# Performance work log

Measured on AMD Instinct MI355X. Metric: run time of the kernel, lower is better.

The kernel has to match this reference:

```python
import jax, jax.numpy as jnp
import numpy as np

EMBD = 256
HEAD = 4
HEAD_DIM = EMBD // HEAD  # 64


def setup_inputs() -> dict:
    key = jax.random.key(0)
    ks = jax.random.split(key, 5)
    B, S = 16, 1024
    scale = 1.0 / np.sqrt(EMBD)
    return {
        "x": jax.random.normal(ks[0], (B, S, EMBD), dtype=jnp.float32),
        "W_qkv": jax.random.normal(ks[1], (EMBD, 3 * EMBD), dtype=jnp.float32) * scale,
        "b_qkv": jax.random.normal(ks[2], (3 * EMBD,), dtype=jnp.float32) * 0.01,
        "W_out": jax.random.normal(ks[3], (EMBD, EMBD), dtype=jnp.float32) * scale,
        "b_out": jax.random.normal(ks[4], (EMBD,), dtype=jnp.float32) * 0.01,
    }


def reference(x, W_qkv, b_qkv, W_out, b_out):
    B, S, E = x.shape
    qkv = x @ W_qkv + b_qkv  # [B,S,3E]
    q, k, v = jnp.split(qkv, 3, axis=-1)
    # [B,S,E] -> [B,H,S,D]
    q = q.reshape(B, S, HEAD, HEAD_DIM).transpose(0, 2, 1, 3)
    k = k.reshape(B, S, HEAD, HEAD_DIM).transpose(0, 2, 1, 3)
    v = v.reshape(B, S, HEAD, HEAD_DIM).transpose(0, 2, 1, 3)
    att = jnp.einsum("bhqd,bhkd->bhqk", q, k) / jnp.sqrt(jnp.float32(HEAD_DIM))
    causal = jnp.tril(jnp.ones((S, S), dtype=bool))
    att = jnp.where(causal, att, -jnp.inf)
    att = jax.nn.softmax(att, axis=-1)
    out = jnp.einsum("bhqk,bhkd->bhqd", att, v)  # [B,H,S,D]
    out = out.transpose(0, 2, 1, 3).reshape(B, S, E)
    return out @ W_out + b_out
```

## Files before the change

kernel.cpp:

```cpp
#include <hip/hip_runtime.h>


typedef unsigned short ushort_t;
typedef __bf16 bf16x8 __attribute__((ext_vector_type(8)));
typedef __bf16 bf16x4 __attribute__((ext_vector_type(4)));
typedef unsigned short u16x8 __attribute__((ext_vector_type(8)));
typedef unsigned short u16x4 __attribute__((ext_vector_type(4)));
typedef float f32x4 __attribute__((ext_vector_type(4)));
typedef short s16x4 __attribute__((ext_vector_type(4)));

__device__ __forceinline__ ushort_t f2bf(float f) {
  __bf16 h = (__bf16)f;
  return __builtin_bit_cast(ushort_t, h);
}

__device__ __forceinline__ void gload_lds16(const ushort_t* g, ushort_t* l) {
  __builtin_amdgcn_global_load_lds(
      (const __attribute__((address_space(1))) unsigned int*)g,
      (__attribute__((address_space(3))) unsigned int*)l, 16, 0, 0);
}

#define BARRIER_RAW() do { __builtin_amdgcn_s_barrier(); \
                           __builtin_amdgcn_sched_barrier(0); } while (0)

__device__ __forceinline__ f32x4 mfma16(bf16x4 a, bf16x4 b, f32x4 c) {
#if __has_builtin(__builtin_amdgcn_mfma_f32_16x16x16bf16_1k)
  return __builtin_amdgcn_mfma_f32_16x16x16bf16_1k(
      __builtin_bit_cast(s16x4, a), __builtin_bit_cast(s16x4, b), c, 0, 0, 0);
#elif __has_builtin(__builtin_amdgcn_mfma_f32_16x16x16_bf16)
  return __builtin_amdgcn_mfma_f32_16x16x16_bf16(a, b, c, 0, 0, 0);
#else
  f32x4 d = c;
  asm volatile("v_mfma_f32_16x16x16_bf16 %0, %1, %2, %0"
               : "+v"(d) : "v"(a), "v"(b));
  return d;
#endif
}

__global__ __launch_bounds__(256)
void convert_all(const float* __restrict__ x,
                 const float* __restrict__ Wq, const float* __restrict__ Wo,
                 ushort_t* __restrict__ xb,
                 ushort_t* __restrict__ WqT, ushort_t* __restrict__ WoT)
{
  int blk = blockIdx.x;
  if (blk < 2048) {
    const int xc = blk & 7, j = blk >> 3;
    const size_t base = (size_t)xc * 524288 + (size_t)j * 2048 + threadIdx.x * 8;
    float4 v0 = *(const float4*)&x[base];
    float4 v1 = *(const float4*)&x[base + 4];
    u16x8 ov;
    ov[0]=f2bf(v0.x); ov[1]=f2bf(v0.y); ov[2]=f2bf(v0.z); ov[3]=f2bf(v0.w);
    ov[4]=f2bf(v1.x); ov[5]=f2bf(v1.y); ov[6]=f2bf(v1.z); ov[7]=f2bf(v1.w);
    *(u16x8*)&xb[base] = ov;
    return;
  }
  blk -= 2048;
  __shared__ float t[64][65];
  const float* src; ushort_t* dst; int ld_src, k0, n0;
  if (blk < 48) { src = Wq; dst = WqT; ld_src = 768;
                  k0 = (blk / 12) * 64; n0 = (blk % 12) * 64; }
  else { blk -= 48; src = Wo; dst = WoT; ld_src = 256;
         k0 = (blk / 4) * 64; n0 = (blk % 4) * 64; }
  const int tr = threadIdx.x >> 6, tc = threadIdx.x & 63;
  #pragma unroll
  for (int i = 0; i < 16; ++i) {
    const int r = i * 4 + tr;
    t[r][tc] = src[(size_t)(k0 + r) * ld_src + n0 + tc];
  }
  __syncthreads();
  #pragma unroll
  for (int i = 0; i < 16; ++i) {
    const int r = i * 4 + tr;
    dst[(size_t)(n0 + r) * 256 + k0 + tc] = f2bf(t[tc][r]);
  }
}

template<int OUT_MODE, int NB>
__global__ __launch_bounds__(256, 2)
void gemm_bias(const ushort_t* __restrict__ A, int ldA,
               const ushort_t* __restrict__ Bt,
               const float* __restrict__ bias,
               void* __restrict__ Outp, int ldOut,
               ushort_t* __restrict__ Vt)
{
  __shared__ ushort_t Bl[64][256];
  __shared__ ushort_t Al[4][3][64][32];

  const int tid = threadIdx.x;
  const int lane = tid & 63;
  const int w  = tid >> 6;
  const int l15 = lane & 15, g = lane >> 4;

  const int nwg = NB * 64;
  const int inner = (int)blockIdx.x % nwg;
  const int chunkXCD = nwg >> 3;
  const int gidx = (inner & 7) * chunkXCD + (inner >> 3);
  const int n0 = (gidx % NB) * 64;
  const int mBase = (gidx / NB) * 256;
  const int mw = mBase + w * 64;
  const bool vmode = (OUT_MODE == 0) && (n0 >= 512);

  #pragma unroll
  for (int i = 0; i < 8; ++i) {
    const int L = i * 256 + tid;
    const int r = L >> 5, c = L & 31;
    gload_lds16(&Bt[(size_t)(n0 + r) * 256 + (c ^ (r & 7)) * 8],
                &Bl[0][0] + (size_t)L * 8);
  }
  #pragma unroll
  for (int s = 0; s < 2; ++s)
    #pragma unroll
    for (int i = 0; i < 4; ++i) {
      const int L = i * 64 + lane;
      const int r = L >> 2, c = L & 3;
      gload_lds16(&A[(size_t)(mw + r) * ldA + s*32 + (c ^ ((r >> 1) & 3)) * 8],
                  &Al[w][s][0][0] + (size_t)L * 8);
    }
  asm volatile("s_waitcnt vmcnt(8)" ::: "memory");
  BARRIER_RAW();

  f32x4 acc[4][4] = {};

  #pragma unroll
  for (int t = 0; t < 8; ++t) {
    if (t < 6) {
      #pragma unroll
      for (int i = 0; i < 4; ++i) {
        const int L = i * 64 + lane;
        const int r = L >> 2, c = L & 3;
        gload_lds16(&A[(size_t)(mw + r) * ldA + (t+2)*32
                       + (c ^ ((r >> 1) & 3)) * 8],
                    &Al[w][(t + 2) % 3][0][0] + (size_t)L * 8);
      }
    }
    if (t < 6)      asm volatile("s_waitcnt vmcnt(8)" ::: "memory");
    else if (t == 6) asm volatile("s_waitcnt vmcnt(4)" ::: "memory");
    else             asm volatile("s_waitcnt vmcnt(0)" ::: "memory");

    bf16x8 af[4], bfr[4];
    #pragma unroll
    for (int mi = 0; mi < 4; ++mi) {
      const int r = mi * 16 + l15;
      af[mi] = __builtin_bit_cast(bf16x8,
          *(const u16x8*)&Al[w][t % 3][r][(g ^ ((r >> 1) & 3)) * 8]);
    }
    #pragma unroll
    for (int ni = 0; ni < 4; ++ni) {
      const int r = ni * 16 + l15;
      bfr[ni] = __builtin_bit_cast(bf16x8,
          *(const u16x8*)&Bl[r][((t*4 + g) ^ (r & 7)) * 8]);
    }
    if (vmode) {
      #pragma unroll
      for (int mi = 0; mi < 4; ++mi)
        #pragma unroll
        for (int ni = 0; ni < 4; ++ni)
          acc[mi][ni] = __builtin_amdgcn_mfma_f32_16x16x32_bf16(
                            bfr[ni], af[mi], acc[mi][ni], 0, 0, 0);
    } else {
      #pragma unroll
      for (int mi = 0; mi < 4; ++mi)
        #pragma unroll
        for (int ni = 0; ni < 4; ++ni)
          acc[mi][ni] = __builtin_amdgcn_mfma_f32_16x16x32_bf16(
                            af[mi], bfr[ni], acc[mi][ni], 0, 0, 0);
    }
  }

  #pragma unroll
  for (int mi = 0; mi < 4; ++mi)
    #pragma unroll
    for (int ni = 0; ni < 4; ++ni) {
      if (!vmode) {
        const int col = n0 + ni * 16 + l15;
        const float bv = bias[col];
        #pragma unroll
        for (int r = 0; r < 4; ++r) {
          const int row = mw + mi * 16 + g * 4 + r;
          const float v = acc[mi][ni][r] + bv;
          if (OUT_MODE == 1)
            ((float*)Outp)[(size_t)row * ldOut + col] = v;
          else
            ((ushort_t*)Outp)[(size_t)row * 512 + col] = f2bf(v);
        }
      } else {
        const int hh = (n0 - 512) >> 6;
        const int m = mw + mi * 16 + l15;
        const int bb = m >> 10, ss = m & 1023;
        ushort_t* vbase =
            &Vt[(size_t)(((bb*4 + hh)*16 + (ss >> 6)) * 4096) + (ss & 63)];
        #pragma unroll
        for (int r = 0; r < 4; ++r) {
          const int nn = n0 + ni * 16 + g * 4 + r;
          const float v = acc[mi][ni][r] + bias[nn];
          vbase[(size_t)((nn - 512) & 63) * 64] = f2bf(v);
        }
      }
    }
}

__global__ __launch_bounds__(256, 2)
void attn_kernel(ushort_t* __restrict__ qk, const ushort_t* __restrict__ Vt)
{
  __shared__ ushort_t K_lds[4][64][64];
  __shared__ ushort_t V_lds[4][64][64];

  const int lid = blockIdx.x;
  const int xc  = lid & 7;
  const int p   = (lid >> 3) & 7;
  const int bhi = lid >> 6;
  const int b   = 2 * xc + (bhi >> 2);
  const int h   = bhi & 3;
  const int bh  = b * 4 + h;
  const int qtA = p, qtB = 15 - p;

  const int tid = threadIdx.x;
  const int lane = tid & 63;
  const int w = tid >> 6;
  const int l15 = lane & 15, g = lane >> 4;

  const size_t rowbase = (size_t)b * 1024;
  const int qc = h * 64, kc = 256 + h * 64;
  const ushort_t* Vtt = Vt + (size_t)bh * 16 * 4096;

  bf16x8 qfA[2], qfB[2];
  {
    const size_t ra = rowbase + qtA*64 + w*16 + l15;
    const size_t rb = rowbase + qtB*64 + w*16 + l15;
    #pragma unroll
    for (int ks = 0; ks < 2; ++ks) {
      qfA[ks] = __builtin_bit_cast(bf16x8,
                  *(const u16x8*)&qk[ra*512 + qc + ks*32 + g*8]);
      qfB[ks] = __builtin_bit_cast(bf16x8,
                  *(const u16x8*)&qk[rb*512 + qc + ks*32 + g*8]);
    }
  }

  f32x4 oA[4] = {}, oB[4] = {};
  float lsA = 0.f, lsB = 0.f;
  const int qgA = qtA*64 + w*16 + l15;
  const int qgB = qtB*64 + w*16 + l15;

  auto stage = [&](int bi, int kt) {
    const int kv0 = kt * 64;
    const ushort_t* vtile = Vtt + kt * 4096;
    #pragma unroll
    for (int ri = 0; ri < 2; ++ri) {
      const int L = ri*256 + tid;
      const int r = L >> 3;
      gload_lds16(&qk[(rowbase + kv0 + r)*512 + kc + ((L & 7) ^ (r & 7))*8],
                  &K_lds[bi][0][0] + (size_t)L*8);
      gload_lds16(&vtile[r*64 + ((L & 7) ^ ((r >> 1) & 7))*8],
                  &V_lds[bi][0][0] + (size_t)L*8);
    }
  };

  stage(0, 0);
  stage(1, 1);
  stage(2, 2);
  asm volatile("s_waitcnt vmcnt(8)" ::: "memory");
  BARRIER_RAW();

  for (int kt = 0; kt <= qtB; ++kt) {
    const int cur = kt & 3;
    stage((kt + 3) & 3, (kt + 3 <= qtB) ? kt + 3 : qtB);

    bf16x8 kf[2][4];
    #pragma unroll
    for (int ks = 0; ks < 2; ++ks)
      #pragma unroll
      for (int ni = 0; ni < 4; ++ni) {
        const int row = ni*16 + l15;
        kf[ks][ni] = __builtin_bit_cast(bf16x8,
            *(const u16x8*)&K_lds[cur][row][(((ks*4 + g) ^ (row & 7))) * 8]);
      }
    bf16x4 vf[4][4];
    #pragma unroll
    for (int ni = 0; ni < 4; ++ni)
      #pragma unroll
      for (int da = 0; da < 4; ++da) {
        const int row = da*16 + l15;
        const int phys = (ni*2 + (g >> 1)) ^ ((row >> 1) & 7);
        vf[ni][da] = __builtin_bit_cast(bf16x4,
            *(const u16x4*)&V_lds[cur][row][phys*8 + (g & 1)*4]);
      }

    const int kv0 = kt * 64;
    const int g4 = g * 4;

    auto tile_step = [&](const bf16x8 (&qf)[2], f32x4 (&o)[4], float &ls,
                         int qg, bool diag) {
      f32x4 s[4] = {};
      #pragma unroll
      for (int ks = 0; ks < 2; ++ks)
        #pragma unroll
        for (int ni = 0; ni < 4; ++ni)
          s[ni] = __builtin_amdgcn_mfma_f32_16x16x32_bf16(kf[ks][ni], qf[ks],
                                                          s[ni], 0, 0, 0);
      bf16x4 pn[4];
      #pragma unroll
      for (int ni = 0; ni < 4; ++ni)
        #pragma unroll
        for (int r = 0; r < 4; ++r) {
          float e = exp2f(fmaf(s[ni][r], 0.18033688011112042f,
                               -14.426950408889634f));
          if (diag) e = (kv0 + ni*16 + g4 + r <= qg) ? e : 0.0f;
          ls += e;
          pn[ni][r] = (__bf16)e;
        }
      #pragma unroll
      for (int ni = 0; ni < 4; ++ni)
        #pragma unroll
        for (int da = 0; da < 4; ++da)
          o[da] = mfma16(vf[ni][da], pn[ni], o[da]);
    };

    tile_step(qfB, oB, lsB, qgB, kt == qtB);
    if (kt <= qtA) tile_step(qfA, oA, lsA, qgA, kt == qtA);

    asm volatile("s_waitcnt vmcnt(8)" ::: "memory");
    BARRIER_RAW();
  }

  asm volatile("s_nop 7\n\ts_nop 7" :::);

  lsA += __shfl_xor(lsA, 16); lsA += __shfl_xor(lsA, 32);
  lsB += __shfl_xor(lsB, 16); lsB += __shfl_xor(lsB, 32);
  const float invA = 1.f / lsA;
  const float invB = 1.f / lsB;

  {
    const size_t rowA = rowbase + (size_t)qgA;
    const size_t rowB = rowbase + (size_t)qgB;
    #pragma unroll
    for (int da = 0; da < 4; ++da) {
      u16x4 ovA, ovB;
      #pragma unroll
      for (int r = 0; r < 4; ++r) {
        ovA[r] = f2bf(oA[da][r] * invA);
        ovB[r] = f2bf(oB[da][r] * invB);
      }
      *(u16x4*)&qk[rowA*512 + qc + da*16 + g*4] = ovA;
      *(u16x4*)&qk[rowB*512 + qc + da*16 + g*4] = ovB;
    }
  }
}

extern "C" void kernel_launch(void* const* d_in, const int* in_sizes, int n_in,
                              void* d_out, int out_size, void* d_ws, size_t ws_size,
                              hipStream_t stream)
{
  const float* x     = (const float*)d_in[0];
  const float* W_qkv = (const float*)d_in[1];
  const float* b_qkv = (const float*)d_in[2];
  const float* W_out = (const float*)d_in[3];
  const float* b_out = (const float*)d_in[4];
  float* out = (float*)d_out;

  char* ws = (char*)d_ws;
  ushort_t* WqT = (ushort_t*)ws;
  ushort_t* WoT = (ushort_t*)(ws + 393216);
  ushort_t* qk  = (ushort_t*)(ws + 524288);
  ushort_t* Vt  = (ushort_t*)(ws + 17301504);
  ushort_t* xb  = (ushort_t*)(ws + 25690112);

  convert_all<<<dim3(2112), dim3(256), 0, stream>>>(x, W_qkv, W_out, xb, WqT, WoT);
  gemm_bias<0, 12><<<dim3(768), dim3(256), 0, stream>>>(
      xb, 256, WqT, b_qkv, qk, 512, Vt);
  attn_kernel<<<dim3(512), dim3(256), 0, stream>>>(qk, Vt);
  gemm_bias<1, 4><<<dim3(256), dim3(256), 0, stream>>>(
      qk, 512, WoT, b_out, out, 256, nullptr);
}
```

Baseline: 63.41 us.

## Fuse fp32-to-bf16 conversion of x into the QKV GEMM A-tile loads

The separate pass that converts the whole x tensor to bf16 is removed. The QKV GEMM now reads fp32 x directly, converts it in registers and writes it into a double-buffered LDS tile, with register prefetch two tiles ahead. The QKV GEMM tile shrinks to 128 rows per block (32 per wave) with occupancy hint 3 and twice as many blocks, to make room for the register staging. This drops one full read and write round trip of x in bf16, but the A path no longer uses direct global-to-LDS loads and now carries more register and wait overhead.

```diff
diff --git a/kernel.cpp b/kernel.cpp
--- a/kernel.cpp
+++ b/kernel.cpp
@@ -38,25 +38,11 @@
 }
 
 __global__ __launch_bounds__(256)
-void convert_all(const float* __restrict__ x,
-                 const float* __restrict__ Wq, const float* __restrict__ Wo,
-                 ushort_t* __restrict__ xb,
-                 ushort_t* __restrict__ WqT, ushort_t* __restrict__ WoT)
+void convert_wt(const float* __restrict__ Wq, const float* __restrict__ Wo,
+                ushort_t* __restrict__ WqT, ushort_t* __restrict__ WoT)
 {
+  __shared__ float t[64][65];
   int blk = blockIdx.x;
-  if (blk < 2048) {
-    const int xc = blk & 7, j = blk >> 3;
-    const size_t base = (size_t)xc * 524288 + (size_t)j * 2048 + threadIdx.x * 8;
-    float4 v0 = *(const float4*)&x[base];
-    float4 v1 = *(const float4*)&x[base + 4];
-    u16x8 ov;
-    ov[0]=f2bf(v0.x); ov[1]=f2bf(v0.y); ov[2]=f2bf(v0.z); ov[3]=f2bf(v0.w);
-    ov[4]=f2bf(v1.x); ov[5]=f2bf(v1.y); ov[6]=f2bf(v1.z); ov[7]=f2bf(v1.w);
-    *(u16x8*)&xb[base] = ov;
-    return;
-  }
-  blk -= 2048;
-  __shared__ float t[64][65];
   const float* src; ushort_t* dst; int ld_src, k0, n0;
   if (blk < 48) { src = Wq; dst = WqT; ld_src = 768;
                   k0 = (blk / 12) * 64; n0 = (blk % 12) * 64; }
@@ -76,30 +62,66 @@
   }
 }
 
-template<int OUT_MODE, int NB>
-__global__ __launch_bounds__(256, 2)
-void gemm_bias(const ushort_t* __restrict__ A, int ldA,
-               const ushort_t* __restrict__ Bt,
-               const float* __restrict__ bias,
-               void* __restrict__ Outp, int ldOut,
-               ushort_t* __restrict__ Vt)
+template<int A_F32, int OUT_MODE, int NB>
+__global__ __launch_bounds__(256, 3)
+void gemm_v5(const void* __restrict__ Ap, int ldA,
+             const ushort_t* __restrict__ Bt,
+             const float* __restrict__ bias,
+             void* __restrict__ Outp, int ldOut,
+             ushort_t* __restrict__ Vt)
 {
   __shared__ ushort_t Bl[64][256];
-  __shared__ ushort_t Al[4][3][64][32];
+  __shared__ ushort_t Al[4][2][32][32];
 
   const int tid = threadIdx.x;
   const int lane = tid & 63;
   const int w  = tid >> 6;
   const int l15 = lane & 15, g = lane >> 4;
 
-  const int nwg = NB * 64;
-  const int inner = (int)blockIdx.x % nwg;
+  const int nwg = NB * 128;
+  const int inner = (int)blockIdx.x;
   const int chunkXCD = nwg >> 3;
   const int gidx = (inner & 7) * chunkXCD + (inner >> 3);
   const int n0 = (gidx % NB) * 64;
-  const int mBase = (gidx / NB) * 256;
-  const int mw = mBase + w * 64;
+  const int mBase = (gidx / NB) * 128;
+  const int mw = mBase + w * 32;
   const bool vmode = (OUT_MODE == 0) && (n0 >= 512);
+
+  const int ar0 = lane >> 2, ar1 = 16 + ar0, ac = lane & 3;
+  const int acc0 = ac ^ ((ar0 >> 1) & 3);
+  const int acc1 = ac ^ ((ar1 >> 1) & 3);
+
+  auto loadA = [&](int t, float4& f0, float4& f1, float4& f2, float4& f3) {
+    if constexpr (A_F32) {
+      const float* Af = (const float*)Ap;
+      const float* p0 = &Af[(size_t)(mw + ar0) * ldA + t*32 + acc0*8];
+      const float* p1 = &Af[(size_t)(mw + ar1) * ldA + t*32 + acc1*8];
+      f0 = *(const float4*)p0; f1 = *(const float4*)(p0 + 4);
+      f2 = *(const float4*)p1; f3 = *(const float4*)(p1 + 4);
+    } else {
+      const ushort_t* Ab = (const ushort_t*)Ap;
+      f0 = *(const float4*)&Ab[(size_t)(mw + ar0) * ldA + t*32 + acc0*8];
+      f2 = *(const float4*)&Ab[(size_t)(mw + ar1) * ldA + t*32 + acc1*8];
+    }
+  };
+  auto writeA = [&](int buf, const float4& f0, const float4& f1,
+                    const float4& f2, const float4& f3) {
+    u16x8 u0, u1;
+    if constexpr (A_F32) {
+      u0[0]=f2bf(f0.x); u0[1]=f2bf(f0.y); u0[2]=f2bf(f0.z); u0[3]=f2bf(f0.w);
+      u0[4]=f2bf(f1.x); u0[5]=f2bf(f1.y); u0[6]=f2bf(f1.z); u0[7]=f2bf(f1.w);
+      u1[0]=f2bf(f2.x); u1[1]=f2bf(f2.y); u1[2]=f2bf(f2.z); u1[3]=f2bf(f2.w);
+      u1[4]=f2bf(f3.x); u1[5]=f2bf(f3.y); u1[6]=f2bf(f3.z); u1[7]=f2bf(f3.w);
+    } else {
+      u0 = __builtin_bit_cast(u16x8, f0);
+      u1 = __builtin_bit_cast(u16x8, f2);
+    }
+    *(u16x8*)&Al[w][buf][ar0][ac*8] = u0;
+    *(u16x8*)&Al[w][buf][ar1][ac*8] = u1;
+  };
+  #define VMCNT_A() do { if constexpr (A_F32) \
+      asm volatile("s_waitcnt vmcnt(4)" ::: "memory"); \
+    else asm volatile("s_waitcnt vmcnt(2)" ::: "memory"); } while (0)
 
   #pragma unroll
   for (int i = 0; i < 8; ++i) {
@@ -108,42 +130,28 @@
     gload_lds16(&Bt[(size_t)(n0 + r) * 256 + (c ^ (r & 7)) * 8],
                 &Bl[0][0] + (size_t)L * 8);
   }
-  #pragma unroll
-  for (int s = 0; s < 2; ++s)
-    #pragma unroll
-    for (int i = 0; i < 4; ++i) {
-      const int L = i * 64 + lane;
-      const int r = L >> 2, c = L & 3;
-      gload_lds16(&A[(size_t)(mw + r) * ldA + s*32 + (c ^ ((r >> 1) & 3)) * 8],
-                  &Al[w][s][0][0] + (size_t)L * 8);
-    }
-  asm volatile("s_waitcnt vmcnt(8)" ::: "memory");
+  float4 a0, a1, a2, a3, b0, b1, b2, b3;
+  loadA(0, a0, a1, a2, a3);
+  loadA(1, b0, b1, b2, b3);
+  VMCNT_A();
+  writeA(0, a0, a1, a2, a3);
+  asm volatile("s_waitcnt lgkmcnt(0)" ::: "memory");
   BARRIER_RAW();
 
-  f32x4 acc[4][4] = {};
+  f32x4 acc[2][4] = {};
 
   #pragma unroll
   for (int t = 0; t < 8; ++t) {
     if (t < 6) {
-      #pragma unroll
-      for (int i = 0; i < 4; ++i) {
-        const int L = i * 64 + lane;
-        const int r = L >> 2, c = L & 3;
-        gload_lds16(&A[(size_t)(mw + r) * ldA + (t+2)*32
-                       + (c ^ ((r >> 1) & 3)) * 8],
-                    &Al[w][(t + 2) % 3][0][0] + (size_t)L * 8);
-      }
-    }
-    if (t < 6)      asm volatile("s_waitcnt vmcnt(8)" ::: "memory");
-    else if (t == 6) asm volatile("s_waitcnt vmcnt(4)" ::: "memory");
-    else             asm volatile("s_waitcnt vmcnt(0)" ::: "memory");
-
-    bf16x8 af[4], bfr[4];
-    #pragma unroll
-    for (int mi = 0; mi < 4; ++mi) {
+      if (t & 1) loadA(t + 2, b0, b1, b2, b3);
+      else       loadA(t + 2, a0, a1, a2, a3);
+    }
+    bf16x8 af[2], bfr[4];
+    #pragma unroll
+    for (int mi = 0; mi < 2; ++mi) {
       const int r = mi * 16 + l15;
       af[mi] = __builtin_bit_cast(bf16x8,
-          *(const u16x8*)&Al[w][t % 3][r][(g ^ ((r >> 1) & 3)) * 8]);
+          *(const u16x8*)&Al[w][t & 1][r][(g ^ ((r >> 1) & 3)) * 8]);
     }
     #pragma unroll
     for (int ni = 0; ni < 4; ++ni) {
@@ -153,23 +161,30 @@
     }
     if (vmode) {
       #pragma unroll
-      for (int mi = 0; mi < 4; ++mi)
+      for (int mi = 0; mi < 2; ++mi)
         #pragma unroll
         for (int ni = 0; ni < 4; ++ni)
           acc[mi][ni] = __builtin_amdgcn_mfma_f32_16x16x32_bf16(
                             bfr[ni], af[mi], acc[mi][ni], 0, 0, 0);
     } else {
       #pragma unroll
-      for (int mi = 0; mi < 4; ++mi)
+      for (int mi = 0; mi < 2; ++mi)
         #pragma unroll
         for (int ni = 0; ni < 4; ++ni)
           acc[mi][ni] = __builtin_amdgcn_mfma_f32_16x16x32_bf16(
                             af[mi], bfr[ni], acc[mi][ni], 0, 0, 0);
     }
-  }
-
-  #pragma unroll
-  for (int mi = 0; mi < 4; ++mi)
+    if (t < 6) VMCNT_A();
+    else if (t == 6) asm volatile("s_waitcnt vmcnt(0)" ::: "memory");
+    if (t < 7) {
+      if (t & 1) writeA((t + 1) & 1, a0, a1, a2, a3);
+      else       writeA((t + 1) & 1, b0, b1, b2, b3);
+      asm volatile("s_waitcnt lgkmcnt(0)" ::: "memory");
+    }
+  }
+
+  #pragma unroll
+  for (int mi = 0; mi < 2; ++mi)
     #pragma unroll
     for (int ni = 0; ni < 4; ++ni) {
       if (!vmode) {
@@ -198,6 +213,131 @@
         }
       }
     }
+  #undef VMCNT_A
+}
+
+template<int OUT_MODE, int NB>
+__global__ __launch_bounds__(256, 2)
+void gemm_v4(const ushort_t* __restrict__ A, int ldA,
+             const ushort_t* __restrict__ Bt,
+             const float* __restrict__ bias,
+             void* __restrict__ Outp, int ldOut,
+             ushort_t* __restrict__ Vt)
+{
+  __shared__ ushort_t Bl[64][256];
+  __shared__ ushort_t Al[4][3][64][32];
+
+  const int tid = threadIdx.x;
+  const int lane = tid & 63;
+  const int w  = tid >> 6;
+  const int l15 = lane & 15, g = lane >> 4;
+
+  const int nwg = NB * 64;
+  const int inner = (int)blockIdx.x % nwg;
+  const int chunkXCD = nwg >> 3;
+  const int gidx = (inner & 7) * chunkXCD + (inner >> 3);
+  const int n0 = (gidx % NB) * 64;
+  const int mBase = (gidx / NB) * 256;
+  const int mw = mBase + w * 64;
+  const bool vmode = (OUT_MODE == 0) && (n0 >= 512);
+
+  #pragma unroll
+  for (int i = 0; i < 8; ++i) {
+    const int L = i * 256 + tid;
+    const int r = L >> 5, c = L & 31;
+    gload_lds16(&Bt[(size_t)(n0 + r) * 256 + (c ^ (r & 7)) * 8],
+                &Bl[0][0] + (size_t)L * 8);
+  }
+  #pragma unroll
+  for (int s = 0; s < 2; ++s)
+    #pragma unroll
+    for (int i = 0; i < 4; ++i) {
+      const int L = i * 64 + lane;
+      const int r = L >> 2, c = L & 3;
+      gload_lds16(&A[(size_t)(mw + r) * ldA + s*32 + (c ^ ((r >> 1) & 3)) * 8],
+                  &Al[w][s][0][0] + (size_t)L * 8);
+    }
+  asm volatile("s_waitcnt vmcnt(8)" ::: "memory");
+  BARRIER_RAW();
+
+  f32x4 acc[4][4] = {};
+
+  #pragma unroll
+  for (int t = 0; t < 8; ++t) {
+    if (t < 6) {
+      #pragma unroll
+      for (int i = 0; i < 4; ++i) {
+        const int L = i * 64 + lane;
+        const int r = L >> 2, c = L & 3;
+        gload_lds16(&A[(size_t)(mw + r) * ldA + (t+2)*32
+                       + (c ^ ((r >> 1) & 3)) * 8],
+                    &Al[w][(t + 2) % 3][0][0] + (size_t)L * 8);
+      }
+    }
+    if (t < 6)      asm volatile("s_waitcnt vmcnt(8)" ::: "memory");
+    else if (t == 6) asm volatile("s_waitcnt vmcnt(4)" ::: "memory");
+    else             asm volatile("s_waitcnt vmcnt(0)" ::: "memory");
+
+    bf16x8 af[4], bfr[4];
+    #pragma unroll
+    for (int mi = 0; mi < 4; ++mi) {
+      const int r = mi * 16 + l15;
+      af[mi] = __builtin_bit_cast(bf16x8,
+          *(const u16x8*)&Al[w][t % 3][r][(g ^ ((r >> 1) & 3)) * 8]);
+    }
+    #pragma unroll
+    for (int ni = 0; ni < 4; ++ni) {
+      const int r = ni * 16 + l15;
+      bfr[ni] = __builtin_bit_cast(bf16x8,
+          *(const u16x8*)&Bl[r][((t*4 + g) ^ (r & 7)) * 8]);
+    }
+    if (vmode) {
+      #pragma unroll
+      for (int mi = 0; mi < 4; ++mi)
+        #pragma unroll
+        for (int ni = 0; ni < 4; ++ni)
+          acc[mi][ni] = __builtin_amdgcn_mfma_f32_16x16x32_bf16(
+                            bfr[ni], af[mi], acc[mi][ni], 0, 0, 0);
+    } else {
+      #pragma unroll
+      for (int mi = 0; mi < 4; ++mi)
+        #pragma unroll
+        for (int ni = 0; ni < 4; ++ni)
+          acc[mi][ni] = __builtin_amdgcn_mfma_f32_16x16x32_bf16(
+                            af[mi], bfr[ni], acc[mi][ni], 0, 0, 0);
+    }
+  }
+
+  #pragma unroll
+  for (int mi = 0; mi < 4; ++mi)
+    #pragma unroll
+    for (int ni = 0; ni < 4; ++ni) {
+      if (!vmode) {
+        const int col = n0 + ni * 16 + l15;
+        const float bv = bias[col];
+        #pragma unroll
+        for (int r = 0; r < 4; ++r) {
+          const int row = mw + mi * 16 + g * 4 + r;
+          const float v = acc[mi][ni][r] + bv;
+          if (OUT_MODE == 1)
+            ((float*)Outp)[(size_t)row * ldOut + col] = v;
+          else
+            ((ushort_t*)Outp)[(size_t)row * 512 + col] = f2bf(v);
+        }
+      } else {
+        const int hh = (n0 - 512) >> 6;
+        const int m = mw + mi * 16 + l15;
+        const int bb = m >> 10, ss = m & 1023;
+        ushort_t* vbase =
+            &Vt[(size_t)(((bb*4 + hh)*16 + (ss >> 6)) * 4096) + (ss & 63)];
+        #pragma unroll
+        for (int r = 0; r < 4; ++r) {
+          const int nn = n0 + ni * 16 + g * 4 + r;
+          const float v = acc[mi][ni][r] + bias[nn];
+          vbase[(size_t)((nn - 512) & 63) * 64] = f2bf(v);
+        }
+      }
+    }
 }
 
 __global__ __launch_bounds__(256, 2)
@@ -363,12 +503,11 @@
   ushort_t* WoT = (ushort_t*)(ws + 393216);
   ushort_t* qk  = (ushort_t*)(ws + 524288);
   ushort_t* Vt  = (ushort_t*)(ws + 17301504);
-  ushort_t* xb  = (ushort_t*)(ws + 25690112);
-
-  convert_all<<<dim3(2112), dim3(256), 0, stream>>>(x, W_qkv, W_out, xb, WqT, WoT);
-  gemm_bias<0, 12><<<dim3(768), dim3(256), 0, stream>>>(
-      xb, 256, WqT, b_qkv, qk, 512, Vt);
+
+  convert_wt<<<dim3(64), dim3(256), 0, stream>>>(W_qkv, W_out, WqT, WoT);
+  gemm_v5<1, 0, 12><<<dim3(1536), dim3(256), 0, stream>>>(
+      x, 256, WqT, b_qkv, qk, 512, Vt);
   attn_kernel<<<dim3(512), dim3(256), 0, stream>>>(qk, Vt);
-  gemm_bias<1, 4><<<dim3(256), dim3(256), 0, stream>>>(
+  gemm_v4<1, 4><<<dim3(256), dim3(256), 0, stream>>>(
       qk, 512, WoT, b_out, out, 256, nullptr);
 }
```

Result: no change. 62.79 us (-1.0%).
